# Performance work log

Hardware: AMD Instinct MI355X
Metric: run time of the kernel (lower is better)

## Reference

```python
import jax, jax.numpy as jnp
import numpy as np

V, T, E, HID = 50000, 32, 256, 512
H = HID // 2  # per-direction LSTM hidden
L, B = 512, 64


def setup_inputs() -> dict:
    key = jax.random.key(0)
    ks = jax.random.split(key, 18)
    p = lambda k, shape: (jax.random.normal(k, shape, jnp.float32) * 0.1)
    return {
        'seqs': jax.random.randint(ks[0], (L, B), 0, V),
        'tags': jax.random.randint(ks[1], (L, B), 0, T),
        'masks': jnp.ones((L, B), jnp.int32),
        'embed_table': p(ks[2], (V, E)),
        'W_ih_f': p(ks[3], (4 * H, E)), 'W_hh_f': p(ks[4], (4 * H, H)),
        'b_ih_f': p(ks[5], (4 * H,)),   'b_hh_f': p(ks[6], (4 * H,)),
        'W_ih_b': p(ks[7], (4 * H, E)), 'W_hh_b': p(ks[8], (4 * H, H)),
        'b_ih_b': p(ks[9], (4 * H,)),   'b_hh_b': p(ks[10], (4 * H,)),
        'W_out': p(ks[11], (T, HID)),   'b_out': p(ks[12], (T,)),
        'start_trans': p(ks[13], (T,)), 'end_trans': p(ks[14], (T,)),
        'trans': p(ks[15], (T, T)),
    }


def _lstm(xs, mask_b, W_ih, W_hh, b_ih, b_hh, reverse):
    # xs: [L,B,E], mask_b: [L,B] bool. Masked updates emulate packed sequences
    # (state frozen and output zeroed at padded steps).
    Bsz = xs.shape[1]
    Hd = W_hh.shape[1]
    x_proj = jnp.einsum('lbe,ge->lbg', xs, W_ih) + b_ih + b_hh  # precompute input gates

    def step(carry, inp):
        h, c = carry
        xg, m = inp
        gates = xg + h @ W_hh.T
        i, f, g, o = jnp.split(gates, 4, axis=-1)  # torch gate order i,f,g,o
        i, f, o = jax.nn.sigmoid(i), jax.nn.sigmoid(f), jax.nn.sigmoid(o)
        g = jnp.tanh(g)
        c_new = f * c + i * g
        h_new = o * jnp.tanh(c_new)
        m = m[:, None]
        h = jnp.where(m, h_new, h)
        c = jnp.where(m, c_new, c)
        out = jnp.where(m, h_new, 0.0)
        return (h, c), out

    init = (jnp.zeros((Bsz, Hd), xs.dtype), jnp.zeros((Bsz, Hd), xs.dtype))
    _, outs = jax.lax.scan(step, init, (x_proj, mask_b), reverse=reverse)
    return outs  # [L,B,H]


def reference(seqs, tags, masks, embed_table,
              W_ih_f, W_hh_f, b_ih_f, b_hh_f,
              W_ih_b, W_hh_b, b_ih_b, b_hh_b,
              W_out, b_out, start_trans, end_trans, trans):
    mb = masks.astype(bool)  # [L,B]
    emb = embed_table[seqs]  # [L,B,E]; dropout is identity in eval mode
    h_f = _lstm(emb, mb, W_ih_f, W_hh_f, b_ih_f, b_hh_f, reverse=False)
    h_b = _lstm(emb, mb, W_ih_b, W_hh_b, b_ih_b, b_hh_b, reverse=True)
    lstm_out = jnp.concatenate([h_f, h_b], axis=-1)           # [L,B,HID]
    emissions = jnp.einsum('lbh,th->lbt', lstm_out, W_out) + b_out  # [L,B,T]

    Lb, Bb = seqs.shape
    mf = masks[1:].astype(emissions.dtype)  # [L-1,B]

    # ---- gold path score (pytorch-crf numerator) ----
    e_scores = jnp.take_along_axis(emissions, tags[:, :, None], axis=2)[:, :, 0]  # [L,B]
    t_scores = trans[tags[:-1], tags[1:]]                                         # [L-1,B]
    lengths = masks.sum(0)
    last_tags = tags[lengths - 1, jnp.arange(Bb)]
    numerator = (start_trans[tags[0]] + e_scores[0]
                 + ((e_scores[1:] + t_scores) * mf).sum(0)
                 + end_trans[last_tags])  # [B]

    # ---- partition function (forward algorithm) ----
    def part_step(score, xs):
        e_t, m_t = xs  # [B,T], [B]
        nxt = jax.nn.logsumexp(score[:, :, None] + trans[None] + e_t[:, None, :], axis=1)
        return jnp.where(m_t[:, None], nxt, score), None

    score0 = start_trans[None, :] + emissions[0]
    score, _ = jax.lax.scan(part_step, score0, (emissions[1:], mb[1:]))
    log_z = jax.nn.logsumexp(score + end_trans[None, :], axis=1)  # [B]

    llh = numerator - log_z
    return -llh.mean()
```

## Files before the change

### kernel.cpp

```cpp
#include <hip/hip_runtime.h>
#include <hip/hip_bf16.h>
#include <stdint.h>

#define DEVINL __device__ __forceinline__

typedef __attribute__((ext_vector_type(8))) short short8;
typedef __attribute__((ext_vector_type(4))) float float4v;


DEVINL float bf2f(short s) {
  union { unsigned u; float f; } v; v.u = ((unsigned)(unsigned short)s) << 16; return v.f;
}
DEVINL unsigned short f2bf(float f) {
  union { float f; unsigned u; } v; v.f = f;
  unsigned r = v.u + 0x7FFFu + ((v.u >> 16) & 1u);
  return (unsigned short)(r >> 16);
}
DEVINL float sigmf(float x) { return __fdividef(1.0f, 1.0f + __expf(-x)); }
DEVINL float tanhf_(float x) {
  x = fminf(20.0f, fmaxf(-20.0f, x));
  float e = __expf(-2.0f * x);
  return __fdividef(1.0f - e, 1.0f + e);
}

__global__ void k_cvt(const float* __restrict__ src, short* __restrict__ dst, int n8) {
  int i = blockIdx.x * blockDim.x + threadIdx.x;
  int stride = gridDim.x * blockDim.x;
  for (; i < n8; i += stride) {
    const float4v* s = (const float4v*)(src + (size_t)i * 8);
    float4v a = s[0], b = s[1];
    short8 o;
    o[0] = (short)f2bf(a[0]); o[1] = (short)f2bf(a[1]);
    o[2] = (short)f2bf(a[2]); o[3] = (short)f2bf(a[3]);
    o[4] = (short)f2bf(b[0]); o[5] = (short)f2bf(b[1]);
    o[6] = (short)f2bf(b[2]); o[7] = (short)f2bf(b[3]);
    ((short8*)dst)[i] = o;
  }
}

__global__ void k_bias(const float* __restrict__ a1, const float* __restrict__ a2,
                       const float* __restrict__ b1, const float* __restrict__ b2,
                       float* __restrict__ o) {
  int i = blockIdx.x * blockDim.x + threadIdx.x;
  o[i] = (i < 1024) ? (a1[i] + a2[i]) : (b1[i - 1024] + b2[i - 1024]);
}

__launch_bounds__(256)
__global__ void k_xproj(const int* __restrict__ seqs, const short* __restrict__ embT,
                        const short* __restrict__ wihX, const float* __restrict__ biasX,
                        short* __restrict__ xproj) {
  __shared__ short As[128 * 256];
  __shared__ short Bs[128 * 256];
  __shared__ int ids[128];
  const int bm = blockIdx.x >> 4, bn = blockIdx.x & 15;
  const int tid = threadIdx.x;
  if (tid < 128) ids[tid] = seqs[bm * 128 + tid];
  __syncthreads();
#pragma unroll
  for (int i = 0; i < 16; ++i) {
    int task = tid + i * 256, row = task >> 5, kc = task & 31;
    short8 v = *(const short8*)(embT + (size_t)ids[row] * 256 + kc * 8);
    *(short8*)((char*)As + row * 512 + ((kc * 16) ^ ((row & 7) << 4))) = v;
  }
#pragma unroll
  for (int i = 0; i < 16; ++i) {
    int task = tid + i * 256, row = task >> 5, kc = task & 31;
    short8 v = *(const short8*)(wihX + (size_t)(bn * 128 + row) * 256 + kc * 8);
    *(short8*)((char*)Bs + row * 512 + ((kc * 16) ^ ((row & 7) << 4))) = v;
  }
  __syncthreads();
  const int wave = tid >> 6, lane = tid & 63, l15 = lane & 15, l4 = lane >> 4;
  float4v acc[2][8];
#pragma unroll
  for (int m = 0; m < 2; ++m)
#pragma unroll
    for (int n = 0; n < 8; ++n) acc[m][n] = (float4v){0.f, 0.f, 0.f, 0.f};
#pragma unroll
  for (int kt = 0; kt < 8; ++kt) {
    const int kb = kt * 64 + l4 * 16;
    short8 a[2], b[8];
#pragma unroll
    for (int m = 0; m < 2; ++m) {
      int row = (wave * 2 + m) * 16 + l15;
      a[m] = *(short8*)((char*)As + row * 512 + (kb ^ ((row & 7) << 4)));
    }
#pragma unroll
    for (int n = 0; n < 8; ++n) {
      int row = n * 16 + l15;
      b[n] = *(short8*)((char*)Bs + row * 512 + (kb ^ ((row & 7) << 4)));
    }
#pragma unroll
    for (int m = 0; m < 2; ++m)
#pragma unroll
      for (int n = 0; n < 8; ++n)
        acc[m][n] = __builtin_amdgcn_mfma_f32_16x16x32_bf16(a[m], b[n], acc[m][n], 0, 0, 0);
  }
#pragma unroll
  for (int n = 0; n < 8; ++n) {
    int col = bn * 128 + n * 16 + l15;
    float bias = biasX[col];
#pragma unroll
    for (int m = 0; m < 2; ++m) {
      int token = bm * 128 + (wave * 2 + m) * 16 + l4 * 4;
#pragma unroll
      for (int q = 0; q < 4; ++q)
        xproj[(size_t)(token + q) * 2048 + col] = (short)f2bf(acc[m][n][q] + bias);
    }
  }
}

__launch_bounds__(256, 1)
__global__ void k_lstm(const short* __restrict__ xproj, const short* __restrict__ whhX,
                       const int* __restrict__ masks, short* __restrict__ h_all,
                       unsigned long long* __restrict__ hX, int* __restrict__ flags) {
  const int wg = blockIdx.x;
  const int dir = wg >> 4, bg = (wg >> 3) & 1, rg = wg & 7, grp = wg >> 3;
  const int tid = threadIdx.x, wave = tid >> 6, lane = tid & 63;
  const int sv = wave >> 1, nt = wave & 1;
  const int l15 = lane & 15, l4 = lane >> 4;
  const int bloc = nt * 16 + l15;
  const int bglob = bg * 32 + bloc;
  const int jbase = sv * 16 + l4 * 4;
  const int kout = rg * 32 + jbase;

  short8 wf[4][8];
#pragma unroll
  for (int g = 0; g < 4; ++g) {
    const short* wrow = whhX + (size_t)(dir * 1024 + g * 256 + rg * 32 + sv * 16 + l15) * 256;
#pragma unroll
    for (int kt = 0; kt < 8; ++kt) wf[g][kt] = *(const short8*)(wrow + kt * 32 + l4 * 8);
  }

  unsigned long long* hXg = hX + (dir * 2 + bg) * 2 * 2048;
  const int wIdx = ((kout >> 3) * 32 + bloc) * 2 + ((kout >> 2) & 1);
  int* flg = flags + grp * 512;

  float c[4] = {0.f, 0.f, 0.f, 0.f}, hq[4] = {0.f, 0.f, 0.f, 0.f};

  int tseq = dir ? 511 : 0;
  unsigned long long xp[4];
#pragma unroll
  for (int g = 0; g < 4; ++g)
    xp[g] = *(const unsigned long long*)(xproj + (size_t)(tseq * 64 + bglob) * 2048 + dir * 1024 + g * 256 + kout);
  int mcur = masks[tseq * 64 + bglob];

#pragma unroll 1
  for (int step = 0; step < 512; ++step) {
    tseq = dir ? (511 - step) : step;
    float4v acc[4];
#pragma unroll
    for (int g = 0; g < 4; ++g) {
      float4v a;
#pragma unroll
      for (int q = 0; q < 4; ++q) a[q] = bf2f((short)(unsigned short)(xp[g] >> (16 * q)));
      acc[g] = a;
    }
    int tn = dir ? (510 - step) : (step + 1);
    tn = tn < 0 ? 0 : (tn > 511 ? 511 : tn);
    unsigned long long xpn[4];
#pragma unroll
    for (int g = 0; g < 4; ++g)
      xpn[g] = *(const unsigned long long*)(xproj + (size_t)(tn * 64 + bglob) * 2048 + dir * 1024 + g * 256 + kout);
    int mn = masks[tn * 64 + bglob];

    if (step > 0) {
      while (__hip_atomic_load(&flg[step - 1], __ATOMIC_RELAXED, __HIP_MEMORY_SCOPE_AGENT) < 8)
        __builtin_amdgcn_s_sleep(1);
      __atomic_signal_fence(__ATOMIC_ACQUIRE);
      unsigned long long* src = hXg + ((step - 1) & 1) * 2048;
      unsigned long long bl[8][2];
#pragma unroll
      for (int kt = 0; kt < 8; ++kt) {
        int base = ((kt * 4 + l4) * 32 + bloc) * 2;
        bl[kt][0] = __hip_atomic_load(src + base,     __ATOMIC_RELAXED, __HIP_MEMORY_SCOPE_AGENT);
        bl[kt][1] = __hip_atomic_load(src + base + 1, __ATOMIC_RELAXED, __HIP_MEMORY_SCOPE_AGENT);
      }
#pragma unroll
      for (int kt = 0; kt < 8; ++kt) {
        union { unsigned long long u[2]; short8 v; } uu;
        uu.u[0] = bl[kt][0]; uu.u[1] = bl[kt][1];
#pragma unroll
        for (int g = 0; g < 4; ++g)
          acc[g] = __builtin_amdgcn_mfma_f32_16x16x32_bf16(wf[g][kt], uu.v, acc[g], 0, 0, 0);
      }
    }

    float outq[4];
#pragma unroll
    for (int q = 0; q < 4; ++q) {
      float iv = sigmf(acc[0][q]);
      float fv = sigmf(acc[1][q]);
      float gv = tanhf_(acc[2][q]);
      float ov = sigmf(acc[3][q]);
      float cn = fv * c[q] + iv * gv;
      float hn = ov * tanhf_(cn);
      c[q]  = mcur ? cn : c[q];
      hq[q] = mcur ? hn : hq[q];
      outq[q] = mcur ? hn : 0.f;
    }
    unsigned long long hp =
        (unsigned long long)f2bf(hq[0]) | ((unsigned long long)f2bf(hq[1]) << 16) |
        ((unsigned long long)f2bf(hq[2]) << 32) | ((unsigned long long)f2bf(hq[3]) << 48);
    unsigned long long op =
        (unsigned long long)f2bf(outq[0]) | ((unsigned long long)f2bf(outq[1]) << 16) |
        ((unsigned long long)f2bf(outq[2]) << 32) | ((unsigned long long)f2bf(outq[3]) << 48);
    __hip_atomic_store(hXg + (step & 1) * 2048 + wIdx, hp, __ATOMIC_RELAXED, __HIP_MEMORY_SCOPE_AGENT);
    *(unsigned long long*)(h_all + (size_t)(tseq * 64 + bglob) * 512 + dir * 256 + kout) = op;
    __syncthreads();
    if (tid == 0)
      __hip_atomic_fetch_add(&flg[step], 1, __ATOMIC_RELAXED, __HIP_MEMORY_SCOPE_AGENT);
#pragma unroll
    for (int g = 0; g < 4; ++g) xp[g] = xpn[g];
    mcur = mn;
  }
}

__launch_bounds__(256)
__global__ void k_emis(const short* __restrict__ h_all, const short* __restrict__ woutX,
                       const float* __restrict__ bout, float* __restrict__ emis) {
  const int tid = threadIdx.x, wave = tid >> 6, lane = tid & 63;
  const int l15 = lane & 15, l4 = lane >> 4;
  const int token0 = blockIdx.x * 256 + wave * 64;
  float4v acc[4][2];
#pragma unroll
  for (int m = 0; m < 4; ++m)
#pragma unroll
    for (int n = 0; n < 2; ++n) acc[m][n] = (float4v){0.f, 0.f, 0.f, 0.f};
#pragma unroll
  for (int kt = 0; kt < 16; ++kt) {
    short8 b[2];
#pragma unroll
    for (int n = 0; n < 2; ++n)
      b[n] = *(const short8*)(woutX + (size_t)(n * 16 + l15) * 512 + kt * 32 + l4 * 8);
#pragma unroll
    for (int m = 0; m < 4; ++m) {
      short8 a = *(const short8*)(h_all + (size_t)(token0 + m * 16 + l15) * 512 + kt * 32 + l4 * 8);
#pragma unroll
      for (int n = 0; n < 2; ++n)
        acc[m][n] = __builtin_amdgcn_mfma_f32_16x16x32_bf16(a, b[n], acc[m][n], 0, 0, 0);
    }
  }
#pragma unroll
  for (int n = 0; n < 2; ++n) {
    float bias = bout[n * 16 + l15];
#pragma unroll
    for (int m = 0; m < 4; ++m) {
      int token = token0 + m * 16 + l4 * 4;
#pragma unroll
      for (int q = 0; q < 4; ++q)
        emis[(size_t)(token + q) * 32 + n * 16 + l15] = acc[m][n][q] + bias;
    }
  }
}

__launch_bounds__(64)
__global__ void k_crf(const float* __restrict__ emis, const int* __restrict__ tags,
                      const int* __restrict__ masks, const float* __restrict__ strans,
                      const float* __restrict__ etrans, const float* __restrict__ trans,
                      float* __restrict__ out) {
  __shared__ float trans_s[1024];
  __shared__ float score_s[32];
  const int b = blockIdx.x, lane = threadIdx.x;
  for (int i = lane; i < 1024; i += 64) trans_s[i] = trans[i];

  float num = 0.f; int lensum = 0;
#pragma unroll 1
  for (int i = 0; i < 8; ++i) {
    int t = lane + i * 64;
    int tg = tags[t * 64 + b];
    int m = masks[t * 64 + b];
    lensum += m;
    float e = emis[(size_t)(t * 64 + b) * 32 + tg];
    if (t == 0) num += strans[tg] + e;
    else if (m) num += e + trans[tags[(t - 1) * 64 + b] * 32 + tg];
  }
#pragma unroll
  for (int o = 32; o > 0; o >>= 1) { num += __shfl_down(num, o); lensum += __shfl_down(lensum, o); }
  num = __shfl(num, 0);
  lensum = __shfl(lensum, 0);
  num += etrans[tags[(lensum - 1) * 64 + b]];
  __syncthreads();

  const int jp = lane & 31, half = lane >> 5;
  if (lane < 32) score_s[jp] = strans[jp] + emis[(size_t)b * 32 + jp];
  __syncthreads();

  float e_next = emis[(size_t)(64 + b) * 32 + jp];
#pragma unroll 1
  for (int t = 1; t < 512; ++t) {
    float e = e_next;
    if (t < 511) e_next = emis[(size_t)((t + 1) * 64 + b) * 32 + jp];
    int m = masks[t * 64 + b];
    float v[16], mx = -1e30f;
#pragma unroll
    for (int j = 0; j < 16; ++j) {
      v[j] = score_s[half * 16 + j] + trans_s[(half * 16 + j) * 32 + jp];
      mx = fmaxf(mx, v[j]);
    }
    float sum = 0.f;
#pragma unroll
    for (int j = 0; j < 16; ++j) sum += __expf(v[j] - mx);
    float mo = __shfl_xor(mx, 32), so = __shfl_xor(sum, 32);
    float mn2 = fmaxf(mx, mo);
    sum = sum * __expf(mx - mn2) + so * __expf(mo - mn2);
    float nxt = e + mn2 + __logf(sum);
    float cur = score_s[jp];
    float ns = m ? nxt : cur;
    __syncthreads();
    if (lane < 32) score_s[jp] = ns;
    __syncthreads();
  }

  float vv = (lane < 32) ? (score_s[jp] + etrans[jp]) : -1e30f;
  float mx = vv;
#pragma unroll
  for (int o = 32; o > 0; o >>= 1) mx = fmaxf(mx, __shfl_xor(mx, o));
  float sm = (lane < 32) ? __expf(vv - mx) : 0.f;
#pragma unroll
  for (int o = 32; o > 0; o >>= 1) sm += __shfl_xor(sm, o);
  float lz = mx + __logf(sm);
  if (lane == 0) atomicAdd(out, -(num - lz) * (1.0f / 64.0f));
}

extern "C" void kernel_launch(void* const* d_in, const int* in_sizes, int n_in,
                              void* d_out, int out_size, void* d_ws, size_t ws_size,
                              hipStream_t stream) {
  const int*   seqs  = (const int*)d_in[0];
  const int*   tags  = (const int*)d_in[1];
  const int*   masks = (const int*)d_in[2];
  const float* embed = (const float*)d_in[3];
  const float* Wihf  = (const float*)d_in[4];
  const float* Whhf  = (const float*)d_in[5];
  const float* bihf  = (const float*)d_in[6];
  const float* bhhf  = (const float*)d_in[7];
  const float* Wihb  = (const float*)d_in[8];
  const float* Whhb  = (const float*)d_in[9];
  const float* bihb  = (const float*)d_in[10];
  const float* bhhb  = (const float*)d_in[11];
  const float* Wout  = (const float*)d_in[12];
  const float* bout  = (const float*)d_in[13];
  const float* strn  = (const float*)d_in[14];
  const float* etrn  = (const float*)d_in[15];
  const float* trn   = (const float*)d_in[16];
  float* outf = (float*)d_out;

  char* ws = (char*)d_ws;
  short* xproj = (short*)(ws + 0);
  short* h_all = (short*)(ws + 134217728);
  float* emis  = (float*)(ws + 167772160);
  short* embT  = (short*)(ws + 171966464);
  short* wihX  = (short*)(ws + 197566464);
  short* whhX  = (short*)(ws + 198615040);
  short* woutX = (short*)(ws + 199663616);
  float* biasX = (float*)(ws + 199696384);
  unsigned long long* hX = (unsigned long long*)(ws + 199704576);
  int* flags = (int*)(ws + 199835648);

  hipMemsetAsync(flags, 0, 8192, stream);
  hipMemsetAsync(d_out, 0, 4, stream);

  k_cvt<<<2048, 256, 0, stream>>>(embed, embT, 1600000);
  k_cvt<<<128, 256, 0, stream>>>(Wihf, wihX, 32768);
  k_cvt<<<128, 256, 0, stream>>>(Wihb, wihX + 262144, 32768);
  k_cvt<<<128, 256, 0, stream>>>(Whhf, whhX, 32768);
  k_cvt<<<128, 256, 0, stream>>>(Whhb, whhX + 262144, 32768);
  k_cvt<<<8, 256, 0, stream>>>(Wout, woutX, 2048);
  k_bias<<<2, 1024, 0, stream>>>(bihf, bhhf, bihb, bhhb, biasX);
  k_xproj<<<4096, 256, 0, stream>>>(seqs, embT, wihX, biasX, xproj);
  k_lstm<<<32, 256, 0, stream>>>(xproj, whhX, masks, h_all, hX, flags);
  k_emis<<<128, 256, 0, stream>>>(h_all, woutX, bout, emis);
  k_crf<<<64, 64, 0, stream>>>(emis, tags, masks, strn, etrn, trn, outf);
}
```

Baseline: 1.985 ms.

## Repartition LSTM recurrence and replace block barrier with per-wave flag sync

Result: slower. 4.051 ms (+104.0%).

```diff
diff --git a/kernel.cpp b/kernel.cpp
--- a/kernel.cpp
+++ b/kernel.cpp
@@ -113,35 +113,36 @@
 __global__ void k_lstm(const short* __restrict__ xproj, const short* __restrict__ whhX,
                        const int* __restrict__ masks, short* __restrict__ h_all,
                        unsigned long long* __restrict__ hX, int* __restrict__ flags) {
-  const int wg = blockIdx.x;
-  const int dir = wg >> 4, bg = (wg >> 3) & 1, rg = wg & 7, grp = wg >> 3;
-  const int tid = threadIdx.x, wave = tid >> 6, lane = tid & 63;
-  const int sv = wave >> 1, nt = wave & 1;
+  const int bid = blockIdx.x;
+  const int gid = bid & 7;
+  const int rg  = bid >> 3;
+  const int dir = gid & 1, bq = gid >> 1;
+  const int tid = threadIdx.x, w = tid >> 6, lane = tid & 63;
   const int l15 = lane & 15, l4 = lane >> 4;
-  const int bloc = nt * 16 + l15;
-  const int bglob = bg * 32 + bloc;
-  const int jbase = sv * 16 + l4 * 4;
-  const int kout = rg * 32 + jbase;
+  const int beta = l15;
+  const int bglob = bq * 16 + beta;
+  const int u0 = rg * 64 + w * 16 + l4 * 4;
 
   short8 wf[4][8];
 #pragma unroll
   for (int g = 0; g < 4; ++g) {
-    const short* wrow = whhX + (size_t)(dir * 1024 + g * 256 + rg * 32 + sv * 16 + l15) * 256;
+    const short* wrow = whhX + (size_t)(dir * 1024 + g * 256 + rg * 64 + w * 16 + l15) * 256;
 #pragma unroll
     for (int kt = 0; kt < 8; ++kt) wf[g][kt] = *(const short8*)(wrow + kt * 32 + l4 * 8);
   }
 
-  unsigned long long* hXg = hX + (dir * 2 + bg) * 2 * 2048;
-  const int wIdx = ((kout >> 3) * 32 + bloc) * 2 + ((kout >> 2) & 1);
-  int* flg = flags + grp * 512;
+  unsigned long long* hbg = hX + (size_t)gid * 2048;
+  int* flg = flags + gid * 16;
+  const int myflag = rg * 4 + w;
 
   float c[4] = {0.f, 0.f, 0.f, 0.f}, hq[4] = {0.f, 0.f, 0.f, 0.f};
 
   int tseq = dir ? 511 : 0;
+  const short* xbase = xproj + dir * 1024 + rg * 64 + w * 16 + l4 * 4;
   unsigned long long xp[4];
 #pragma unroll
   for (int g = 0; g < 4; ++g)
-    xp[g] = *(const unsigned long long*)(xproj + (size_t)(tseq * 64 + bglob) * 2048 + dir * 1024 + g * 256 + kout);
+    xp[g] = *(const unsigned long long*)(xbase + (size_t)(tseq * 64 + bglob) * 2048 + g * 256);
   int mcur = masks[tseq * 64 + bglob];
 
 #pragma unroll 1
@@ -160,20 +161,24 @@
     unsigned long long xpn[4];
 #pragma unroll
     for (int g = 0; g < 4; ++g)
-      xpn[g] = *(const unsigned long long*)(xproj + (size_t)(tn * 64 + bglob) * 2048 + dir * 1024 + g * 256 + kout);
+      xpn[g] = *(const unsigned long long*)(xbase + (size_t)(tn * 64 + bglob) * 2048 + g * 256);
     int mn = masks[tn * 64 + bglob];
 
     if (step > 0) {
-      while (__hip_atomic_load(&flg[step - 1], __ATOMIC_RELAXED, __HIP_MEMORY_SCOPE_AGENT) < 8)
-        __builtin_amdgcn_s_sleep(1);
+      int ready;
+      do {
+        ready = 1;
+#pragma unroll
+        for (int i = 0; i < 16; ++i)
+          ready &= (__hip_atomic_load(&flg[i], __ATOMIC_RELAXED, __HIP_MEMORY_SCOPE_AGENT) >= step) ? 1 : 0;
+      } while (!ready);
       __atomic_signal_fence(__ATOMIC_ACQUIRE);
-      unsigned long long* src = hXg + ((step - 1) & 1) * 2048;
+      const unsigned long long* src = hbg + ((step - 1) & 1) * 1024 + beta * 64;
       unsigned long long bl[8][2];
 #pragma unroll
       for (int kt = 0; kt < 8; ++kt) {
-        int base = ((kt * 4 + l4) * 32 + bloc) * 2;
-        bl[kt][0] = __hip_atomic_load(src + base,     __ATOMIC_RELAXED, __HIP_MEMORY_SCOPE_AGENT);
-        bl[kt][1] = __hip_atomic_load(src + base + 1, __ATOMIC_RELAXED, __HIP_MEMORY_SCOPE_AGENT);
+        bl[kt][0] = __hip_atomic_load(src + kt * 8 + l4 * 2,     __ATOMIC_RELAXED, __HIP_MEMORY_SCOPE_AGENT);
+        bl[kt][1] = __hip_atomic_load(src + kt * 8 + l4 * 2 + 1, __ATOMIC_RELAXED, __HIP_MEMORY_SCOPE_AGENT);
       }
 #pragma unroll
       for (int kt = 0; kt < 8; ++kt) {
@@ -204,11 +209,10 @@
     unsigned long long op =
         (unsigned long long)f2bf(outq[0]) | ((unsigned long long)f2bf(outq[1]) << 16) |
         ((unsigned long long)f2bf(outq[2]) << 32) | ((unsigned long long)f2bf(outq[3]) << 48);
-    __hip_atomic_store(hXg + (step & 1) * 2048 + wIdx, hp, __ATOMIC_RELAXED, __HIP_MEMORY_SCOPE_AGENT);
-    *(unsigned long long*)(h_all + (size_t)(tseq * 64 + bglob) * 512 + dir * 256 + kout) = op;
-    __syncthreads();
-    if (tid == 0)
-      __hip_atomic_fetch_add(&flg[step], 1, __ATOMIC_RELAXED, __HIP_MEMORY_SCOPE_AGENT);
+    __hip_atomic_store(hbg + (step & 1) * 1024 + beta * 64 + (u0 >> 2), hp,
+                       __ATOMIC_RELAXED, __HIP_MEMORY_SCOPE_AGENT);
+    __hip_atomic_store(&flg[myflag], step + 1, __ATOMIC_RELEASE, __HIP_MEMORY_SCOPE_AGENT);
+    *(unsigned long long*)(h_all + (size_t)(tseq * 64 + bglob) * 512 + dir * 256 + u0) = op;
 #pragma unroll
     for (int g = 0; g < 4; ++g) xp[g] = xpn[g];
     mcur = mn;
```
